# Kernel optimization log

Measured on AMD Instinct MI355X. Metric: run time of the kernel, lower is better.

The kernel has to match this reference:

```python
import jax, jax.numpy as jnp
import numpy as np

B, N, C_IN = 128, 49, 2048   # batch, spatial tokens, backbone channels
G, D, H = 256, 768, 8        # query groups, decoder dim, heads
FF = 2048                    # feedforward dim
NUM_CLASSES = 12547
DUP = 50                     # int(12547/256 + 0.999)


def setup_inputs() -> dict:
    key = jax.random.key(0)
    ks = jax.random.split(key, 24)

    def rn(k, shape, std):
        return jax.random.normal(k, shape, dtype=jnp.float32) * std

    inp = {
        "x": rn(ks[0], (B, N, C_IN), 1.0),
        # embed_standart: Linear(2048 -> 768)
        "W_embed": rn(ks[1], (C_IN, D), (2.0 / (C_IN + D)) ** 0.5),
        "b_embed": jnp.zeros((D,), jnp.float32),
        # query embedding (frozen nn.Embedding weight)
        "query": rn(ks[2], (G, D), 1.0),
        # cross-attention projections (MultiheadAttention, 8 heads)
        "Wq": rn(ks[3], (D, D), D ** -0.5), "bq": jnp.zeros((D,), jnp.float32),
        "Wk": rn(ks[4], (D, D), D ** -0.5), "bk": jnp.zeros((D,), jnp.float32),
        "Wv": rn(ks[5], (D, D), D ** -0.5), "bv": jnp.zeros((D,), jnp.float32),
        "Wo": rn(ks[6], (D, D), D ** -0.5), "bo": jnp.zeros((D,), jnp.float32),
        # layer norms
        "g1": jnp.ones((D,), jnp.float32), "beta1": jnp.zeros((D,), jnp.float32),
        "g2": jnp.ones((D,), jnp.float32), "beta2": jnp.zeros((D,), jnp.float32),
        "g3": jnp.ones((D,), jnp.float32), "beta3": jnp.zeros((D,), jnp.float32),
        # FFN
        "W1": rn(ks[7], (D, FF), (2.0 / (D + FF)) ** 0.5), "b1": jnp.zeros((FF,), jnp.float32),
        "W2": rn(ks[8], (FF, D), (2.0 / (D + FF)) ** 0.5), "b2": jnp.zeros((D,), jnp.float32),
        # GroupFC: 256 stacked [768, 50] xavier-normal matrices + class bias
        "Wg": rn(ks[9], (G, D, DUP), (2.0 / (D + DUP)) ** 0.5),
        "bg": jnp.zeros((NUM_CLASSES,), jnp.float32),
    }
    return inp


def _layer_norm(x, g, b, eps=1e-5):
    m = x.mean(-1, keepdims=True)
    v = ((x - m) ** 2).mean(-1, keepdims=True)
    return (x - m) * jax.lax.rsqrt(v + eps) * g + b


def reference(x, W_embed, b_embed, query, Wq, bq, Wk, bk, Wv, bv, Wo, bo,
              g1, beta1, g2, beta2, g3, beta3, W1, b1, W2, b2, Wg, bg):
    hd = D // H
    # embed_standart + relu  -> memory [B, N, D]
    mem = jax.nn.relu(jnp.einsum('bnc,cd->bnd', x, W_embed) + b_embed)
    bs = x.shape[0]
    tgt = jnp.broadcast_to(query[None], (bs, G, D))

    # TransformerDecoderLayerOptimal (eval mode, dropout=identity):
    # tgt = norm1(tgt + dropout1(tgt)) == norm1(2*tgt)
    t = _layer_norm(tgt + tgt, g1, beta1)

    # cross-attention over memory
    q = (t @ Wq + bq).reshape(bs, G, H, hd)
    k = (mem @ Wk + bk).reshape(bs, N, H, hd)
    v = (mem @ Wv + bv).reshape(bs, N, H, hd)
    scores = jnp.einsum('bghd,bnhd->bhgn', q, k) / jnp.asarray(hd, t.dtype) ** 0.5
    attn = jax.nn.softmax(scores, axis=-1)
    o = jnp.einsum('bhgn,bnhd->bghd', attn, v).reshape(bs, G, D)
    o = o @ Wo + bo
    t = _layer_norm(t + o, g2, beta2)

    # FFN
    ff = jax.nn.relu(t @ W1 + b1) @ W2 + b2
    h = _layer_norm(t + ff, g3, beta3)  # [B, G, D]

    # GroupFC: fused grouped GEMM instead of the 256-iteration Python loop
    out_extrap = jnp.einsum('bgd,gdf->bgf', h, Wg)  # [B, G, DUP]
    logits = out_extrap.reshape(bs, G * DUP)[:, :NUM_CLASSES] + bg
    return logits
```

## Files before the change

### kernel.cpp

```cpp
#include <hip/hip_runtime.h>

#define Bn    128
#define Ntok  49
#define CIN   2048
#define Gq    256
#define Dm    768
#define Hh    8
#define HDd   96
#define FFd   2048
#define NCLS  12547
#define DUPn  50

typedef __attribute__((ext_vector_type(8))) short short8;
typedef __attribute__((ext_vector_type(4))) short short4v;
typedef __attribute__((ext_vector_type(4))) float floatx4;

__device__ __forceinline__ unsigned short f2bf(float f) {
  unsigned u = __builtin_bit_cast(unsigned, f);
  u += 0x7fffu + ((u >> 16) & 1u);
  return (unsigned short)(u >> 16);
}
__device__ __forceinline__ float bf2f(unsigned short h) {
  return __builtin_bit_cast(float, (unsigned)h << 16);
}

__device__ __forceinline__ void gl_lds16(const unsigned short* g, unsigned short* l) {
  __builtin_amdgcn_global_load_lds(
      (__attribute__((address_space(1))) void*)g,
      (__attribute__((address_space(3))) void*)l, 16, 0, 0);
}

__global__ __launch_bounds__(256)
void gemm_bt(const unsigned short* __restrict__ A,
             const unsigned short* __restrict__ Bt,
             const float* __restrict__ bias,
             unsigned short* __restrict__ C,
             int M, int N, int K, int relu)
{
  __shared__ unsigned short As[128 * 64];
  __shared__ unsigned short Bs[128 * 64];

  const int tid  = threadIdx.x;
  const int m0   = blockIdx.y << 7;
  const int n0   = blockIdx.x << 7;
  const int wave = tid >> 6, lane = tid & 63;
  const int wm   = (wave >> 1) << 6;
  const int wn   = (wave & 1) << 6;
  const int l16  = lane & 15, quad = lane >> 4;

  const int srow = (wave << 5) + (lane >> 3);
  const int scol = (lane & 7) << 3;
  const unsigned short* gA = A  + (size_t)(m0 + srow) * K + scol;
  const unsigned short* gB = Bt + (size_t)(n0 + srow) * K + scol;
  const size_t rstep8 = (size_t)8 * K;
  unsigned short* lA = &As[(wave << 5) * 64];
  unsigned short* lB = &Bs[(wave << 5) * 64];

  floatx4 acc[4][4];
  const floatx4 zero4 = {0.f, 0.f, 0.f, 0.f};
#pragma unroll
  for (int i = 0; i < 4; ++i)
#pragma unroll
    for (int j = 0; j < 4; ++j) acc[i][j] = zero4;

  for (int k0 = 0; k0 < K; k0 += 64) {
#pragma unroll
    for (int p = 0; p < 4; ++p) {
      gl_lds16(gA + k0 + p * rstep8, lA + (p << 9));
      gl_lds16(gB + k0 + p * rstep8, lB + (p << 9));
    }
    __syncthreads();

#pragma unroll
    for (int ks = 0; ks < 2; ++ks) {
      short8 a[4], b[4];
#pragma unroll
      for (int i = 0; i < 4; ++i)
        a[i] = *(const short8*)&As[(wm + (i << 4) + l16) * 64 + (ks << 5) + (quad << 3)];
#pragma unroll
      for (int j = 0; j < 4; ++j)
        b[j] = *(const short8*)&Bs[(wn + (j << 4) + l16) * 64 + (ks << 5) + (quad << 3)];
#pragma unroll
      for (int i = 0; i < 4; ++i)
#pragma unroll
        for (int j = 0; j < 4; ++j)
          acc[i][j] = __builtin_amdgcn_mfma_f32_16x16x32_bf16(a[i], b[j], acc[i][j], 0, 0, 0);
    }
    __syncthreads();
  }

#pragma unroll
  for (int j = 0; j < 4; ++j) {
    const int col = n0 + wn + (j << 4) + l16;
    const float bv = bias[col];
#pragma unroll
    for (int i = 0; i < 4; ++i) {
      const int rbase = m0 + wm + (i << 4) + (quad << 2);
#pragma unroll
      for (int r = 0; r < 4; ++r) {
        float v = acc[i][j][r] + bv;
        if (relu) v = fmaxf(v, 0.f);
        C[(size_t)(rbase + r) * N + col] = f2bf(v);
      }
    }
  }
}

__global__ __launch_bounds__(256)
void cvt_k(const float* __restrict__ in, unsigned short* __restrict__ out, int n4)
{
  const int i = blockIdx.x * 256 + threadIdx.x;
  if (i < n4) {
    floatx4 v = ((const floatx4*)in)[i];
    short4v s;
    s.x = (short)f2bf(v.x); s.y = (short)f2bf(v.y);
    s.z = (short)f2bf(v.z); s.w = (short)f2bf(v.w);
    ((short4v*)out)[i] = s;
  }
}

struct WPrep {
  const float* src[7];
  unsigned short* dst[7];
  int K[7], N[7], nb[7];
};

__global__ __launch_bounds__(256)
void wprep_k(WPrep p)
{
  __shared__ float tile[32][33];
  int id = blockIdx.x, e = 0, base = 0;
  while (e < 7 && id >= base + p.nb[e]) { base += p.nb[e]; ++e; }
  if (e >= 7) return;
  const int local = id - base;
  const int K = p.K[e], N = p.N[e];
  const int nbx = N >> 5;
  const int nb = (local % nbx) << 5, kb = (local / nbx) << 5;
  const float* in = p.src[e];
  unsigned short* out = p.dst[e];
  const int tx = threadIdx.x & 31, ty = threadIdx.x >> 5;
#pragma unroll
  for (int i = 0; i < 4; ++i)
    tile[ty + (i << 3)][tx] = in[(size_t)(kb + ty + (i << 3)) * N + nb + tx];
  __syncthreads();
#pragma unroll
  for (int i = 0; i < 4; ++i)
    out[(size_t)(nb + ty + (i << 3)) * K + kb + tx] = f2bf(tile[tx][ty + (i << 3)]);
}

__global__ __launch_bounds__(256)
void bkv_k(const float* __restrict__ bk, const float* __restrict__ bv,
           float* __restrict__ o)
{
  const int i = blockIdx.x * 256 + threadIdx.x;
  if (i < Dm) o[i] = bk[i];
  else if (i < 2 * Dm) o[i] = bv[i - Dm];
}

__global__ __launch_bounds__(256)
void wg_trans_k(const float* __restrict__ Wg, unsigned short* __restrict__ out)
{
  __shared__ float tile[32][33];
  const int g  = blockIdx.z;
  const int nb = blockIdx.x << 5, kb = blockIdx.y << 5;
  const int tx = threadIdx.x & 31, ty = threadIdx.x >> 5;
  const float* in = Wg + (size_t)g * Dm * DUPn;
#pragma unroll
  for (int i = 0; i < 4; ++i) {
    const int f = nb + tx;
    tile[ty + (i << 3)][tx] =
        (f < DUPn) ? in[(size_t)(kb + ty + (i << 3)) * DUPn + f] : 0.f;
  }
  __syncthreads();
  unsigned short* o = out + (size_t)g * 64 * Dm;
#pragma unroll
  for (int i = 0; i < 4; ++i)
    o[(size_t)(nb + ty + (i << 3)) * Dm + kb + tx] = f2bf(tile[tx][ty + (i << 3)]);
}

__global__ __launch_bounds__(256)
void groupfc_k(const unsigned short* __restrict__ hb, const unsigned short* __restrict__ wgT,
               const float* __restrict__ bg, float* __restrict__ out,
               int b0, int bcnt)
{
  __shared__ unsigned short As[128 * 32];
  __shared__ unsigned short Bs[64 * 32];

  const int g    = blockIdx.x;
  const int tid  = threadIdx.x;
  const int wave = tid >> 6, lane = tid & 63;
  const int wm   = (wave & 1) << 6;
  const int wn   = (wave >> 1) << 5;
  const int l16  = lane & 15, quad = lane >> 4;

  const int srow = (wave << 5) + (lane >> 2);
  const int brow = (wave << 4) + (lane >> 2);
  const int scol = (lane & 3) << 3;
  const unsigned short* gA = hb + ((size_t)srow * Gq + g) * Dm + scol;
  const unsigned short* gB = wgT + (size_t)g * 64 * Dm + (size_t)brow * Dm + scol;
  const size_t rstepA = (size_t)16 * Gq * Dm;
  unsigned short* lA = &As[wave << 10];
  unsigned short* lB = &Bs[wave << 9];

  floatx4 acc[4][2];
  const floatx4 zero4 = {0.f, 0.f, 0.f, 0.f};
#pragma unroll
  for (int i = 0; i < 4; ++i)
#pragma unroll
    for (int j = 0; j < 2; ++j) acc[i][j] = zero4;

  for (int k0 = 0; k0 < Dm; k0 += 32) {
    gl_lds16(gA + k0,          lA);
    gl_lds16(gA + k0 + rstepA, lA + 512);
    gl_lds16(gB + k0,          lB);
    __syncthreads();

    short8 a[4], b[2];
#pragma unroll
    for (int i = 0; i < 4; ++i)
      a[i] = *(const short8*)&As[(wm + (i << 4) + l16) * 32 + (quad << 3)];
#pragma unroll
    for (int j = 0; j < 2; ++j)
      b[j] = *(const short8*)&Bs[(wn + (j << 4) + l16) * 32 + (quad << 3)];
#pragma unroll
    for (int i = 0; i < 4; ++i)
#pragma unroll
      for (int j = 0; j < 2; ++j)
        acc[i][j] = __builtin_amdgcn_mfma_f32_16x16x32_bf16(a[i], b[j], acc[i][j], 0, 0, 0);
    __syncthreads();
  }

#pragma unroll
  for (int j = 0; j < 2; ++j) {
    const int f = wn + (j << 4) + l16;
    const int col = g * DUPn + f;
    const bool okf = (f < DUPn) && (col < NCLS);
    const float bv = okf ? bg[col] : 0.f;
#pragma unroll
    for (int i = 0; i < 4; ++i) {
      const int bb = wm + (i << 4) + (quad << 2);
#pragma unroll
      for (int r = 0; r < 4; ++r) {
        if (okf && bb + r < bcnt)
          out[(size_t)(b0 + bb + r) * NCLS + col] = acc[i][j][r] + bv;
      }
    }
  }
}

__global__ __launch_bounds__(256)
void ln_query_k(const float* __restrict__ query, const float* __restrict__ gamma,
                const float* __restrict__ beta, unsigned short* __restrict__ out)
{
  const unsigned row = blockIdx.x;
  const float* p = query + (size_t)row * Dm;
  const int tid = threadIdx.x;

  float v[3];
#pragma unroll
  for (int i = 0; i < 3; ++i) v[i] = 2.f * p[tid + (i << 8)];

  float s1 = v[0] + v[1] + v[2];
  float s2 = v[0]*v[0] + v[1]*v[1] + v[2]*v[2];
#pragma unroll
  for (int off = 32; off; off >>= 1) {
    s1 += __shfl_down(s1, off, 64);
    s2 += __shfl_down(s2, off, 64);
  }
  __shared__ float r1[4], r2[4];
  const int wave = tid >> 6, lane = tid & 63;
  if (lane == 0) { r1[wave] = s1; r2[wave] = s2; }
  __syncthreads();
  s1 = r1[0] + r1[1] + r1[2] + r1[3];
  s2 = r2[0] + r2[1] + r2[2] + r2[3];
  const float mean = s1 * (1.f / Dm);
  const float var  = s2 * (1.f / Dm) - mean * mean;
  const float inv  = rsqrtf(var + 1e-5f);
#pragma unroll
  for (int i = 0; i < 3; ++i) {
    const int c = tid + (i << 8);
    out[(size_t)row * Dm + c] = f2bf((v[i] - mean) * inv * gamma[c] + beta[c]);
  }
}

__global__ __launch_bounds__(256)
void ln_k(const unsigned short* __restrict__ in1, const unsigned short* __restrict__ in2,
          unsigned in2mask, const float* __restrict__ gamma,
          const float* __restrict__ beta, unsigned short* __restrict__ out)
{
  const unsigned row = blockIdx.x;
  const unsigned short* p1 = in1 + (size_t)row * Dm;
  const unsigned short* p2 = in2 + (size_t)(row & in2mask) * Dm;
  const int tid = threadIdx.x;

  float v[3];
#pragma unroll
  for (int i = 0; i < 3; ++i) v[i] = bf2f(p1[tid + (i << 8)]) + bf2f(p2[tid + (i << 8)]);

  float s1 = v[0] + v[1] + v[2];
  float s2 = v[0]*v[0] + v[1]*v[1] + v[2]*v[2];
#pragma unroll
  for (int off = 32; off; off >>= 1) {
    s1 += __shfl_down(s1, off, 64);
    s2 += __shfl_down(s2, off, 64);
  }
  __shared__ float r1[4], r2[4];
  const int wave = tid >> 6, lane = tid & 63;
  if (lane == 0) { r1[wave] = s1; r2[wave] = s2; }
  __syncthreads();
  s1 = r1[0] + r1[1] + r1[2] + r1[3];
  s2 = r2[0] + r2[1] + r2[2] + r2[3];
  const float mean = s1 * (1.f / Dm);
  const float var  = s2 * (1.f / Dm) - mean * mean;
  const float inv  = rsqrtf(var + 1e-5f);
#pragma unroll
  for (int i = 0; i < 3; ++i) {
    const int c = tid + (i << 8);
    out[(size_t)row * Dm + c] = f2bf((v[i] - mean) * inv * gamma[c] + beta[c]);
  }
}

__global__ __launch_bounds__(256)
void attn_k(const unsigned short* __restrict__ qall, const unsigned short* __restrict__ kv,
            unsigned short* __restrict__ attno, int b0)
{
  __shared__ unsigned short smem[24576];
  unsigned short* Vt = smem;
  unsigned short* Ks = smem + 6144;
  unsigned short* Ps = smem + 6144;

  const int h = blockIdx.x, bl = blockIdx.y;
  const int b = b0 + bl;
  const int tid  = threadIdx.x;
  const int wave = tid >> 6, lane = tid & 63;
  const int l16  = lane & 15, quad = lane >> 4;
  const int wm   = wave << 6;

  const size_t kvbase = (size_t)b * Ntok * 1536 + h * HDd;

  for (int s = tid; s < 64 * 12; s += 256) {
    const int n = s / 12, c8 = (s - n * 12) << 3;
    short8 v = {0, 0, 0, 0, 0, 0, 0, 0};
    if (n < Ntok) v = *(const short8*)(kv + kvbase + (size_t)n * 1536 + c8);
    *(short8*)&Ks[n * 96 + c8] = v;
  }
  for (int s = tid; s < Ntok * 12; s += 256) {
    const int n = s / 12, c8 = (s - n * 12) << 3;
    short8 v = *(const short8*)(kv + kvbase + (size_t)n * 1536 + Dm + c8);
#pragma unroll
    for (int j = 0; j < 8; ++j) Vt[(c8 + j) * 64 + n] = v[j];
  }
  for (int s = tid; s < 96 * 15; s += 256) {
    const int d = s / 15, n = Ntok + (s - d * 15);
    Vt[d * 64 + n] = 0;
  }
  __syncthreads();

  floatx4 acc[4][4];
  const floatx4 zero4 = {0.f, 0.f, 0.f, 0.f};
#pragma unroll
  for (int i = 0; i < 4; ++i)
#pragma unroll
    for (int j = 0; j < 4; ++j) acc[i][j] = zero4;

#pragma unroll
  for (int kk = 0; kk < 96; kk += 32) {
    short8 a[4], bf[4];
#pragma unroll
    for (int i = 0; i < 4; ++i)
      a[i] = *(const short8*)(qall + (size_t)(wm + (i << 4) + l16) * Dm + h * HDd + kk + (quad << 3));
#pragma unroll
    for (int j = 0; j < 4; ++j)
      bf[j] = *(const short8*)&Ks[((j << 4) + l16) * 96 + kk + (quad << 3)];
#pragma unroll
    for (int i = 0; i < 4; ++i)
#pragma unroll
      for (int j = 0; j < 4; ++j)
        acc[i][j] = __builtin_amdgcn_mfma_f32_16x16x32_bf16(a[i], bf[j], acc[i][j], 0, 0, 0);
  }
  __syncthreads();

  const float scale = 0.10206207261596575f;
#pragma unroll
  for (int i = 0; i < 4; ++i) {
#pragma unroll
    for (int r = 0; r < 4; ++r) {
      float s0 = acc[i][0][r], s1 = acc[i][1][r];
      float s2 = acc[i][2][r], s3 = acc[i][3][r];
      if (l16 > 0) s3 = -1e30f;
      float mx = fmaxf(fmaxf(s0, s1), fmaxf(s2, s3));
      mx = fmaxf(mx, __shfl_xor(mx, 1));
      mx = fmaxf(mx, __shfl_xor(mx, 2));
      mx = fmaxf(mx, __shfl_xor(mx, 4));
      mx = fmaxf(mx, __shfl_xor(mx, 8));
      const float e0 = __expf((s0 - mx) * scale);
      const float e1 = __expf((s1 - mx) * scale);
      const float e2 = __expf((s2 - mx) * scale);
      const float e3 = __expf((s3 - mx) * scale);
      float sum = e0 + e1 + e2 + e3;
      sum += __shfl_xor(sum, 1);
      sum += __shfl_xor(sum, 2);
      sum += __shfl_xor(sum, 4);
      sum += __shfl_xor(sum, 8);
      const float rs = 1.f / sum;
      const int m = wm + (i << 4) + (quad << 2) + r;
      Ps[m * 72 +      l16] = f2bf(e0 * rs);
      Ps[m * 72 + 16 + l16] = f2bf(e1 * rs);
      Ps[m * 72 + 32 + l16] = f2bf(e2 * rs);
      Ps[m * 72 + 48 + l16] = f2bf(e3 * rs);
    }
  }
  __syncthreads();

  floatx4 o[4][6];
#pragma unroll
  for (int i = 0; i < 4; ++i)
#pragma unroll
    for (int j = 0; j < 6; ++j) o[i][j] = zero4;

#pragma unroll
  for (int kk = 0; kk < 64; kk += 32) {
    short8 a[4], bf[6];
#pragma unroll
    for (int i = 0; i < 4; ++i)
      a[i] = *(const short8*)&Ps[(wm + (i << 4) + l16) * 72 + kk + (quad << 3)];
#pragma unroll
    for (int j = 0; j < 6; ++j)
      bf[j] = *(const short8*)&Vt[((j << 4) + l16) * 64 + kk + (quad << 3)];
#pragma unroll
    for (int i = 0; i < 4; ++i)
#pragma unroll
      for (int j = 0; j < 6; ++j)
        o[i][j] = __builtin_amdgcn_mfma_f32_16x16x32_bf16(a[i], bf[j], o[i][j], 0, 0, 0);
  }

#pragma unroll
  for (int j = 0; j < 6; ++j) {
    const int d = (j << 4) + l16;
#pragma unroll
    for (int i = 0; i < 4; ++i) {
      const int mb = wm + (i << 4) + (quad << 2);
#pragma unroll
      for (int r = 0; r < 4; ++r)
        attno[((size_t)bl * Gq + mb + r) * Dm + h * HDd + d] = f2bf(o[i][j][r]);
    }
  }
}


static inline void gemm_launch(const unsigned short* A, const unsigned short* Bt,
                               const float* bias, unsigned short* C,
                               int M, int N, int K, int relu, hipStream_t s) {
  dim3 grid(N >> 7, M >> 7);
  gemm_bt<<<grid, 256, 0, s>>>(A, Bt, bias, C, M, N, K, relu);
}

extern "C" void kernel_launch(void* const* d_in, const int* in_sizes, int n_in,
                              void* d_out, int out_size, void* d_ws, size_t ws_size,
                              hipStream_t stream) {
  const float* x       = (const float*)d_in[0];
  const float* W_embed = (const float*)d_in[1];
  const float* b_embed = (const float*)d_in[2];
  const float* query   = (const float*)d_in[3];
  const float* Wq = (const float*)d_in[4];  const float* bq  = (const float*)d_in[5];
  const float* Wk = (const float*)d_in[6];  const float* bk  = (const float*)d_in[7];
  const float* Wv = (const float*)d_in[8];  const float* bv  = (const float*)d_in[9];
  const float* Wo = (const float*)d_in[10]; const float* bo  = (const float*)d_in[11];
  const float* g1 = (const float*)d_in[12]; const float* be1 = (const float*)d_in[13];
  const float* g2 = (const float*)d_in[14]; const float* be2 = (const float*)d_in[15];
  const float* g3 = (const float*)d_in[16]; const float* be3 = (const float*)d_in[17];
  const float* W1 = (const float*)d_in[18]; const float* b1  = (const float*)d_in[19];
  const float* W2 = (const float*)d_in[20]; const float* b2  = (const float*)d_in[21];
  const float* Wg = (const float*)d_in[22]; const float* bg  = (const float*)d_in[23];
  float* out = (float*)d_out;

  unsigned short* ws    = (unsigned short*)d_ws;
  unsigned short* tbuf  = ws;
  unsigned short* qall  = tbuf  + 196608;
  unsigned short* mem   = qall  + 196608;
  unsigned short* kvbuf = mem   + 4816896;
  unsigned short* xbf   = kvbuf + 9633792;
  unsigned short* wembT = xbf   + 12845056;
  unsigned short* wqT   = wembT + 1572864;
  unsigned short* wkT   = wqT   + 589824;
  unsigned short* wvT   = wkT   + 589824;
  unsigned short* woT   = wvT   + 589824;
  unsigned short* w1T   = woT   + 589824;
  unsigned short* w2T   = w1T   + 1572864;
  float*          bkv   = (float*)(w2T + 1572864);
  unsigned short* attc  = w2T   + 1572864 + 3072;
  unsigned short* wgT   = xbf;

  const size_t fixed_elems = 34769920;
  int CB = 128;
  while (CB > 4 && (fixed_elems + (size_t)CB * 1114112) * 2 > ws_size) CB >>= 1;
  const size_t cstride = (size_t)CB * 196608;
  unsigned short* oprc = attc + cstride;
  unsigned short* t2c  = oprc + cstride;
  unsigned short* ff1c = t2c  + cstride;
  unsigned short* ff2c = attc;
  unsigned short* hc   = oprc;

  cvt_k<<<(Bn * Ntok * CIN / 4 + 255) / 256, 256, 0, stream>>>(x, xbf, Bn * Ntok * CIN / 4);
  {
    WPrep p;
    p.src[0] = W_embed; p.dst[0] = wembT; p.K[0] = CIN; p.N[0] = Dm;
    p.src[1] = Wq;      p.dst[1] = wqT;   p.K[1] = Dm;  p.N[1] = Dm;
    p.src[2] = Wk;      p.dst[2] = wkT;   p.K[2] = Dm;  p.N[2] = Dm;
    p.src[3] = Wv;      p.dst[3] = wvT;   p.K[3] = Dm;  p.N[3] = Dm;
    p.src[4] = Wo;      p.dst[4] = woT;   p.K[4] = Dm;  p.N[4] = Dm;
    p.src[5] = W1;      p.dst[5] = w1T;   p.K[5] = Dm;  p.N[5] = FFd;
    p.src[6] = W2;      p.dst[6] = w2T;   p.K[6] = FFd; p.N[6] = Dm;
    int total = 0;
    for (int e = 0; e < 7; ++e) { p.nb[e] = (p.N[e] >> 5) * (p.K[e] >> 5); total += p.nb[e]; }
    wprep_k<<<total, 256, 0, stream>>>(p);
  }
  bkv_k<<<6, 256, 0, stream>>>(bk, bv, bkv);

  ln_query_k<<<Gq, 256, 0, stream>>>(query, g1, be1, tbuf);
  gemm_launch(tbuf, wqT, bq, qall, Gq, Dm, Dm, 0, stream);
  gemm_launch(xbf, wembT, b_embed, mem, Bn * Ntok, Dm, CIN, 1, stream);
  wg_trans_k<<<dim3(2, Dm / 32, 251), 256, 0, stream>>>(Wg, wgT);
  gemm_launch(mem, wkT, bkv, kvbuf, Bn * Ntok, 2 * Dm, Dm, 0, stream);

  for (int b0 = 0; b0 < Bn; b0 += CB) {
    const int rows = CB * Gq;
    attn_k<<<dim3(Hh, CB), 256, 0, stream>>>(qall, kvbuf, attc, b0);
    gemm_launch(attc, woT, bo, oprc, rows, Dm, Dm, 0, stream);
    ln_k<<<rows, 256, 0, stream>>>(oprc, tbuf, 255u, g2, be2, t2c);
    gemm_launch(t2c, w1T, b1, ff1c, rows, FFd, Dm, 1, stream);
    gemm_launch(ff1c, w2T, b2, ff2c, rows, Dm, FFd, 0, stream);
    ln_k<<<rows, 256, 0, stream>>>(ff2c, t2c, 0xFFFFFFFFu, g3, be3, hc);
    groupfc_k<<<251, 256, 0, stream>>>(hc, wgT, bg, out, b0, CB);
  }
}
```

Measured before the change: 858.2 us.

## Add grouped block swizzle to GEMM and halve K-tile to 32

The GEMM grid becomes 1D, and block indices are remapped into groups of 16 M-tiles so that concurrently running blocks share A/B tiles in L2. The K step per iteration shrinks from 64 to 32, halving LDS use per block, which may raise occupancy. The cost is twice as many __syncthreads barriers and loop iterations, with fewer MFMAs between them to hide load latency.

```diff
diff --git a/kernel.cpp b/kernel.cpp
--- a/kernel.cpp
+++ b/kernel.cpp
@@ -35,26 +35,33 @@
              const unsigned short* __restrict__ Bt,
              const float* __restrict__ bias,
              unsigned short* __restrict__ C,
-             int M, int N, int K, int relu)
-{
-  __shared__ unsigned short As[128 * 64];
-  __shared__ unsigned short Bs[128 * 64];
+             int N, int K, int relu, int gx, int gy)
+{
+  __shared__ unsigned short As[128 * 32];
+  __shared__ unsigned short Bs[128 * 32];
+
+  const int bid = blockIdx.x;
+  const int nig = gx << 4;
+  const int grp = bid / nig;
+  const int rem = bid - grp * nig;
+  const int base_m = grp << 4;
+  int mrows = gy - base_m; if (mrows > 16) mrows = 16;
+  const int m0 = (base_m + rem % mrows) << 7;
+  const int n0 = (rem / mrows) << 7;
 
   const int tid  = threadIdx.x;
-  const int m0   = blockIdx.y << 7;
-  const int n0   = blockIdx.x << 7;
   const int wave = tid >> 6, lane = tid & 63;
   const int wm   = (wave >> 1) << 6;
   const int wn   = (wave & 1) << 6;
   const int l16  = lane & 15, quad = lane >> 4;
 
-  const int srow = (wave << 5) + (lane >> 3);
-  const int scol = (lane & 7) << 3;
+  const int srow = (wave << 5) + (lane >> 2);
+  const int scol = (lane & 3) << 3;
   const unsigned short* gA = A  + (size_t)(m0 + srow) * K + scol;
   const unsigned short* gB = Bt + (size_t)(n0 + srow) * K + scol;
-  const size_t rstep8 = (size_t)8 * K;
-  unsigned short* lA = &As[(wave << 5) * 64];
-  unsigned short* lB = &Bs[(wave << 5) * 64];
+  const size_t rstep = (size_t)16 * K;
+  unsigned short* lA = &As[wave << 10];
+  unsigned short* lB = &Bs[wave << 10];
 
   floatx4 acc[4][4];
   const floatx4 zero4 = {0.f, 0.f, 0.f, 0.f};
@@ -63,29 +70,25 @@
 #pragma unroll
     for (int j = 0; j < 4; ++j) acc[i][j] = zero4;
 
-  for (int k0 = 0; k0 < K; k0 += 64) {
-#pragma unroll
-    for (int p = 0; p < 4; ++p) {
-      gl_lds16(gA + k0 + p * rstep8, lA + (p << 9));
-      gl_lds16(gB + k0 + p * rstep8, lB + (p << 9));
-    }
+  for (int k0 = 0; k0 < K; k0 += 32) {
+    gl_lds16(gA + k0,         lA);
+    gl_lds16(gA + k0 + rstep, lA + 512);
+    gl_lds16(gB + k0,         lB);
+    gl_lds16(gB + k0 + rstep, lB + 512);
     __syncthreads();
 
-#pragma unroll
-    for (int ks = 0; ks < 2; ++ks) {
-      short8 a[4], b[4];
-#pragma unroll
-      for (int i = 0; i < 4; ++i)
-        a[i] = *(const short8*)&As[(wm + (i << 4) + l16) * 64 + (ks << 5) + (quad << 3)];
+    short8 a[4], b[4];
+#pragma unroll
+    for (int i = 0; i < 4; ++i)
+      a[i] = *(const short8*)&As[(wm + (i << 4) + l16) * 32 + (quad << 3)];
+#pragma unroll
+    for (int j = 0; j < 4; ++j)
+      b[j] = *(const short8*)&Bs[(wn + (j << 4) + l16) * 32 + (quad << 3)];
+#pragma unroll
+    for (int i = 0; i < 4; ++i)
 #pragma unroll
       for (int j = 0; j < 4; ++j)
-        b[j] = *(const short8*)&Bs[(wn + (j << 4) + l16) * 64 + (ks << 5) + (quad << 3)];
-#pragma unroll
-      for (int i = 0; i < 4; ++i)
-#pragma unroll
-        for (int j = 0; j < 4; ++j)
-          acc[i][j] = __builtin_amdgcn_mfma_f32_16x16x32_bf16(a[i], b[j], acc[i][j], 0, 0, 0);
-    }
+        acc[i][j] = __builtin_amdgcn_mfma_f32_16x16x32_bf16(a[i], b[j], acc[i][j], 0, 0, 0);
     __syncthreads();
   }
 
@@ -451,8 +454,8 @@
 static inline void gemm_launch(const unsigned short* A, const unsigned short* Bt,
                                const float* bias, unsigned short* C,
                                int M, int N, int K, int relu, hipStream_t s) {
-  dim3 grid(N >> 7, M >> 7);
-  gemm_bt<<<grid, 256, 0, s>>>(A, Bt, bias, C, M, N, K, relu);
+  const int gx = N >> 7, gy = M >> 7;
+  gemm_bt<<<gx * gy, 256, 0, s>>>(A, Bt, bias, C, N, K, relu, gx, gy);
 }
 
 extern "C" void kernel_launch(void* const* d_in, const int* in_sizes, int n_in,
```

Measured after the change: 769.7 us. 10.3% less time.
